# Kernel tuning notes

Measured on AMD Instinct MI355X. Metric: run time of the kernel, lower is better.

## Reference

```python
import jax, jax.numpy as jnp
import numpy as np

N_NODES = 50000
N_EDGES = 1600000
NODE_IN = 128
EDGE_IN = 16
HID = 64

def _glorot(key, shape):
    fan_in = shape[1]
    return jax.random.normal(key, shape, dtype=jnp.float32) / jnp.sqrt(jnp.float32(fan_in))

def setup_inputs() -> dict:
    key = jax.random.key(0)
    ks = jax.random.split(key, 12)
    x = jax.random.normal(ks[0], (N_NODES, NODE_IN), dtype=jnp.float32)
    edge_index = jax.random.randint(ks[1], (2, N_EDGES), 0, N_NODES, dtype=jnp.int64)
    edge_attr = jax.random.normal(ks[2], (N_EDGES, EDGE_IN), dtype=jnp.float32)
    # SAGEConv1: lin_l (neighbor aggr, with bias) and lin_r (root, no bias)
    W1l = _glorot(ks[3], (NODE_IN, HID)); b1l = jnp.zeros((HID,), jnp.float32)
    W1r = _glorot(ks[4], (NODE_IN, HID))
    # SAGEConv2
    W2l = _glorot(ks[5], (HID, HID)); b2l = jnp.zeros((HID,), jnp.float32)
    W2r = _glorot(ks[6], (HID, HID))
    # edge MLP: Linear(2*HID+EDGE_IN, HID) -> ReLU -> Linear(HID, 1)
    Wm1 = _glorot(ks[7], (2 * HID + EDGE_IN, HID)); bm1 = jnp.zeros((HID,), jnp.float32)
    Wm2 = _glorot(ks[8], (HID, 1)); bm2 = jnp.zeros((1,), jnp.float32)
    return {"x": x, "edge_attr": edge_attr,
            "W1l": W1l, "b1l": b1l, "W1r": W1r,
            "W2l": W2l, "b2l": b2l, "W2r": W2r,
            "Wm1": Wm1, "bm1": bm1, "Wm2": Wm2, "bm2": bm2,
            "edge_index": edge_index}

def _sage_conv(h, src, dst, Wl, bl, Wr, n_nodes):
    # mean aggregation of source-node messages at destination nodes
    agg = jax.ops.segment_sum(h[src], dst, num_segments=n_nodes)  # [N, d]
    deg = jax.ops.segment_sum(jnp.ones((src.shape[0],), h.dtype), dst, num_segments=n_nodes)
    mean = agg / jnp.maximum(deg, 1.0)[:, None]
    return mean @ Wl + bl + h @ Wr

def reference(x, edge_attr, W1l, b1l, W1r, W2l, b2l, W2r, Wm1, bm1, Wm2, bm2, edge_index):
    src, dst = edge_index[0], edge_index[1]
    n = x.shape[0]
    h = jax.nn.relu(_sage_conv(x, src, dst, W1l, b1l, W1r, n))
    h = jax.nn.relu(_sage_conv(h, src, dst, W2l, b2l, W2r, n))
    ef = jnp.concatenate([h[src], h[dst], edge_attr], axis=1)  # [E, 2*HID+EDGE_IN]
    hid = jax.nn.relu(ef @ Wm1 + bm1)
    out = hid @ Wm2 + bm2  # [E, 1]
    return jax.nn.sigmoid(out)[:, 0]
```

## Files before the change

### kernel.cpp

```cpp
#include <hip/hip_runtime.h>
#include <hip/hip_bf16.h>
#include <math.h>

#define N_NODES 50000
#define N_EDGES 1600000
#define NODE_IN 128
#define HID 64
#define NODEF (N_NODES * HID)
#define EBLK 64
#define MM1_BLOCKS 1563
#define DEG_BLOCKS 6250
#define NWIN 4
#define SCAN_BLOCKS 49

typedef __hip_bfloat16 bf16;
typedef _Float16 half2t __attribute__((ext_vector_type(2)));

__device__ __forceinline__ float bf2f(bf16 v) { return __bfloat162float(v); }
__device__ __forceinline__ bf16 f2bf(float v) { return __float2bfloat16(v); }

__global__ __launch_bounds__(256) void deg_count_i(const int* __restrict__ dst,
                                                   int* __restrict__ degi, int E) {
    int e = blockIdx.x * blockDim.x + threadIdx.x;
    if (e < E) atomicAdd(&degi[dst[e]], 1);
}

__global__ __launch_bounds__(1024) void scan_blocks(const int* __restrict__ degi,
                                                    int* __restrict__ partial) {
    __shared__ int wsum[16];
    const int t = threadIdx.x;
    const int i = blockIdx.x * 1024 + t;
    const int lane = t & 63, w = t >> 6;
    int v = (i < N_NODES) ? degi[i] : 0;
#pragma unroll
    for (int d = 32; d; d >>= 1) v += __shfl_xor(v, d, 64);
    if (lane == 0) wsum[w] = v;
    __syncthreads();
    if (t == 0) {
        int s = 0;
#pragma unroll
        for (int k = 0; k < 16; ++k) s += wsum[k];
        partial[blockIdx.x] = s;
    }
}

__global__ __launch_bounds__(64) void scan_tops(const int* __restrict__ partial,
                                                int* __restrict__ base) {
    const int t = threadIdx.x;
    int v = (t < SCAN_BLOCKS) ? partial[t] : 0;
    int inc = v;
#pragma unroll
    for (int d = 1; d < 64; d <<= 1) {
        int u = __shfl_up(inc, d, 64);
        if (t >= d) inc += u;
    }
    if (t < SCAN_BLOCKS) base[t] = inc - v;
}

__global__ __launch_bounds__(1024) void scan_final(const int* __restrict__ degi,
                                                   const int* __restrict__ base,
                                                   int* __restrict__ off,
                                                   int* __restrict__ cursor) {
    __shared__ int wsum[16];
    const int t = threadIdx.x;
    const int i = blockIdx.x * 1024 + t;
    const int lane = t & 63, w = t >> 6;
    int v = (i < N_NODES) ? degi[i] : 0;
    int inc = v;
#pragma unroll
    for (int d = 1; d < 64; d <<= 1) {
        int u = __shfl_up(inc, d, 64);
        if (lane >= d) inc += u;
    }
    if (lane == 63) wsum[w] = inc;
    __syncthreads();
    if (w == 0) {
        int s = (lane < 16) ? wsum[lane] : 0;
#pragma unroll
        for (int d = 1; d < 16; d <<= 1) {
            int u = __shfl_up(s, d, 64);
            if (lane >= d) s += u;
        }
        if (lane < 16) wsum[lane] = s;
    }
    __syncthreads();
    const int wbase = (w > 0) ? wsum[w - 1] : 0;
    const int excl = base[blockIdx.x] + wbase + inc - v;
    if (i < N_NODES) { off[i] = excl; cursor[i] = excl; }
    if (i == N_NODES) off[i] = excl;
}

__global__ __launch_bounds__(256) void conv1_fill(const float* __restrict__ in,
                                                  const float* __restrict__ Wa,
                                                  const float* __restrict__ Wb,
                                                  bf16* __restrict__ out1,
                                                  float* __restrict__ out2,
                                                  const int* __restrict__ src,
                                                  const int* __restrict__ dst,
                                                  int* __restrict__ cursor,
                                                  int* __restrict__ csr, int N) {
    constexpr int K = 128, ROWS = 32, PAD = 36;
    __shared__ float xs[K * PAD];
    const int bid = blockIdx.x;
    if (bid >= MM1_BLOCKS) {
        int fb = bid - MM1_BLOCKS;
        int w = fb / DEG_BLOCKS;
        int chunk = fb % DEG_BLOCKS;
        int e = chunk * 256 + threadIdx.x;
        int d = dst[e];
        int lo = w * (N_NODES / NWIN);
        int hi = lo + (N_NODES / NWIN);
        if (d >= lo && d < hi) {
            int p = atomicAdd(&cursor[d], 1);
            csr[p] = src[e];
        }
        return;
    }
    const int row0 = bid * ROWS;
    const int ty = threadIdx.x >> 6;
    const int col = threadIdx.x & 63;
    for (int i = threadIdx.x; i < ROWS * K; i += 256) {
        int r = i / K, c = i % K;
        int row = row0 + r;
        xs[c * PAD + r] = (row < N) ? in[(size_t)row * K + c] : 0.f;
    }
    __syncthreads();
    float a1[8], a2[8];
#pragma unroll
    for (int m = 0; m < 8; ++m) { a1[m] = 0.f; a2[m] = 0.f; }
#pragma unroll 4
    for (int k = 0; k < K; ++k) {
        const float4* xr = (const float4*)(xs + k * PAD + ty * 8);
        float4 xa = xr[0], xb = xr[1];
        float wa = Wa[k * 64 + col];
        float wb = Wb[k * 64 + col];
        a1[0] = fmaf(xa.x, wa, a1[0]); a2[0] = fmaf(xa.x, wb, a2[0]);
        a1[1] = fmaf(xa.y, wa, a1[1]); a2[1] = fmaf(xa.y, wb, a2[1]);
        a1[2] = fmaf(xa.z, wa, a1[2]); a2[2] = fmaf(xa.z, wb, a2[2]);
        a1[3] = fmaf(xa.w, wa, a1[3]); a2[3] = fmaf(xa.w, wb, a2[3]);
        a1[4] = fmaf(xb.x, wa, a1[4]); a2[4] = fmaf(xb.x, wb, a2[4]);
        a1[5] = fmaf(xb.y, wa, a1[5]); a2[5] = fmaf(xb.y, wb, a2[5]);
        a1[6] = fmaf(xb.z, wa, a1[6]); a2[6] = fmaf(xb.z, wb, a2[6]);
        a1[7] = fmaf(xb.w, wa, a1[7]); a2[7] = fmaf(xb.w, wb, a2[7]);
    }
#pragma unroll
    for (int m = 0; m < 8; ++m) {
        int row = row0 + ty * 8 + m;
        if (row < N) {
            unsigned idx = ((unsigned)row << 6) + col;
            out1[idx] = f2bf(a1[m]);
            out2[idx] = a2[m];
        }
    }
}

template <bool OUT1_BF, bool OUT2_BF>
__global__ __launch_bounds__(256) void gather_mm(const bf16* __restrict__ y,
                                                 const float* __restrict__ r,
                                                 const int* __restrict__ csr,
                                                 const int* __restrict__ off,
                                                 const float* __restrict__ bias,
                                                 const float* __restrict__ Wa,
                                                 const float* __restrict__ Wb,
                                                 void* __restrict__ out1v,
                                                 void* __restrict__ out2v, int N) {
    constexpr int K = 64, ROWS = 16, PAD = 20, IDXCAP = 256;
    __shared__ float xs[K * PAD];
    __shared__ int   idx_s[4][IDXCAP];
    const int row0 = blockIdx.x * ROWS;
    const int j  = threadIdx.x & 63;
    const int wv = threadIdx.x >> 6;
    const float bj = bias[j];

    const int nbase = row0 + wv * 4;
    int offs[5];
#pragma unroll
    for (int i = 0; i < 5; ++i) offs[i] = off[nbase + i];
    const int segS = offs[0];
    const int len = offs[4] - segS;
    int* idx_w = idx_s[wv];
    const bool useLds = (len <= IDXCAP);
    if (useLds) {
        for (int i = j; i < len; i += 64)
            idx_w[i] = csr[segS + i];
    }

    for (int m = 0; m < 4; ++m) {
        int lr = wv * 4 + m;
        int node = row0 + lr;
        float acc = 0.f;
        int deg = offs[m + 1] - offs[m];
        if (useLds) {
            int k = offs[m] - segS, s1 = offs[m + 1] - segS;
            for (; k + 15 < s1; k += 16) {
                int sidx[16];
#pragma unroll
                for (int u = 0; u < 16; ++u) sidx[u] = idx_w[k + u];
                float v[16];
#pragma unroll
                for (int u = 0; u < 16; ++u) v[u] = bf2f(y[((unsigned)sidx[u] << 6) + j]);
                float s = 0.f;
#pragma unroll
                for (int u = 0; u < 16; ++u) s += v[u];
                acc += s;
            }
            for (; k + 3 < s1; k += 4) {
                int sa = idx_w[k], sb = idx_w[k + 1], sc = idx_w[k + 2], sd = idx_w[k + 3];
                float va = bf2f(y[((unsigned)sa << 6) + j]);
                float vb = bf2f(y[((unsigned)sb << 6) + j]);
                float vc = bf2f(y[((unsigned)sc << 6) + j]);
                float vd = bf2f(y[((unsigned)sd << 6) + j]);
                acc += (va + vb) + (vc + vd);
            }
            for (; k < s1; ++k)
                acc += bf2f(y[((unsigned)idx_w[k] << 6) + j]);
        } else {
            int k = offs[m], s1 = offs[m + 1];
            for (; k + 15 < s1; k += 16) {
                int sidx[16];
#pragma unroll
                for (int u = 0; u < 16; ++u) sidx[u] = csr[k + u];
                float v[16];
#pragma unroll
                for (int u = 0; u < 16; ++u) v[u] = bf2f(y[((unsigned)sidx[u] << 6) + j]);
                float s = 0.f;
#pragma unroll
                for (int u = 0; u < 16; ++u) s += v[u];
                acc += s;
            }
            for (; k + 3 < s1; k += 4) {
                int sa = csr[k], sb = csr[k + 1], sc = csr[k + 2], sd = csr[k + 3];
                float va = bf2f(y[((unsigned)sa << 6) + j]);
                float vb = bf2f(y[((unsigned)sb << 6) + j]);
                float vc = bf2f(y[((unsigned)sc << 6) + j]);
                float vd = bf2f(y[((unsigned)sd << 6) + j]);
                acc += (va + vb) + (vc + vd);
            }
            for (; k < s1; ++k)
                acc += bf2f(y[((unsigned)csr[k] << 6) + j]);
        }
        float mean = acc / fmaxf((float)deg, 1.f);
        float val = fmaxf(mean + bj + r[((unsigned)node << 6) + j], 0.f);
        xs[j * PAD + lr] = val;
    }
    __syncthreads();

    float a1[4], a2[4];
#pragma unroll
    for (int m = 0; m < 4; ++m) { a1[m] = 0.f; a2[m] = 0.f; }
#pragma unroll 4
    for (int k = 0; k < K; ++k) {
        const float4 xa = *(const float4*)(xs + k * PAD + wv * 4);
        float wa = Wa[k * 64 + j];
        float wb = Wb[k * 64 + j];
        a1[0] = fmaf(xa.x, wa, a1[0]); a2[0] = fmaf(xa.x, wb, a2[0]);
        a1[1] = fmaf(xa.y, wa, a1[1]); a2[1] = fmaf(xa.y, wb, a2[1]);
        a1[2] = fmaf(xa.z, wa, a1[2]); a2[2] = fmaf(xa.z, wb, a2[2]);
        a1[3] = fmaf(xa.w, wa, a1[3]); a2[3] = fmaf(xa.w, wb, a2[3]);
    }
#pragma unroll
    for (int m = 0; m < 4; ++m) {
        int row = row0 + wv * 4 + m;
        if (row < N) {
            unsigned idx = ((unsigned)row << 6) + j;
            if (OUT1_BF) ((bf16*)out1v)[idx] = f2bf(a1[m]);
            else         ((float*)out1v)[idx] = a1[m];
            if (OUT2_BF) ((bf16*)out2v)[idx] = f2bf(a2[m]);
            else         ((float*)out2v)[idx] = a2[m];
        }
    }
}

__device__ __forceinline__ float merge_pair(float lo, float hi, int o, bool bit) {
    float keep = bit ? hi : lo;
    float send = bit ? lo : hi;
    return keep + __shfl_xor(send, o, 64);
}

__global__ __launch_bounds__(256) void edge_fused(const bf16* __restrict__ aE,
                                                  const bf16* __restrict__ bE,
                                                  const float* __restrict__ ea,
                                                  const float* __restrict__ Wbot,
                                                  const float* __restrict__ bm1,
                                                  const float* __restrict__ wm2,
                                                  const float* __restrict__ bm2,
                                                  const int* __restrict__ src,
                                                  const int* __restrict__ dst,
                                                  float* __restrict__ out) {
    __shared__ unsigned ea_s[EBLK * 8];
    __shared__ int      sd_s[2 * EBLK];
    const int t   = threadIdx.x;
    const int eb0 = blockIdx.x * EBLK;
    const int j   = t & 63;
    const int wv  = t >> 6;

    {
        const float2* eaf2 = (const float2*)(ea + (size_t)eb0 * 16);
        for (int i = t; i < EBLK * 8; i += 256) {
            float2 f = eaf2[i];
            half2t p;
            p.x = (_Float16)f.x;
            p.y = (_Float16)f.y;
            ea_s[i] = __builtin_bit_cast(unsigned, p);
        }
    }
    if (t < 2 * EBLK)
        sd_s[t] = (t < EBLK) ? src[eb0 + t] : dst[eb0 + t - EBLK];

    half2t wh[8];
#pragma unroll
    for (int kk = 0; kk < 8; ++kk) {
        wh[kk].x = (_Float16)Wbot[(2 * kk) * 64 + j];
        wh[kk].y = (_Float16)Wbot[(2 * kk + 1) * 64 + j];
    }
    const float bm1c = bm1[j];
    const float wm2c = wm2[j];
    const float bm2c = bm2[0];
    const bool b5 = (j & 32) != 0, b4 = (j & 16) != 0, b3 = (j & 8) != 0;
    __syncthreads();

    const ushort* aU = (const ushort*)aE;
    const ushort* bU = (const ushort*)bE;

    for (int g = 0; g < 2; ++g) {
        const int ebase = wv * 16 + g * 8;
        ushort av[8], bv[8];
#pragma unroll
        for (int u = 0; u < 8; ++u) {
            int e = ebase + u;
            av[u] = aU[((unsigned)sd_s[e] << 6) + j];
            bv[u] = bU[((unsigned)sd_s[EBLK + e] << 6) + j];
        }
        float p[8];
#pragma unroll
        for (int u = 0; u < 8; ++u) {
            const uint4* er = (const uint4*)(ea_s + (ebase + u) * 8);
            uint4 qa = er[0], qb = er[1];
            float v = bm1c;
            v = __builtin_amdgcn_fdot2(__builtin_bit_cast(half2t, qa.x), wh[0], v, false);
            v = __builtin_amdgcn_fdot2(__builtin_bit_cast(half2t, qa.y), wh[1], v, false);
            v = __builtin_amdgcn_fdot2(__builtin_bit_cast(half2t, qa.z), wh[2], v, false);
            v = __builtin_amdgcn_fdot2(__builtin_bit_cast(half2t, qa.w), wh[3], v, false);
            v = __builtin_amdgcn_fdot2(__builtin_bit_cast(half2t, qb.x), wh[4], v, false);
            v = __builtin_amdgcn_fdot2(__builtin_bit_cast(half2t, qb.y), wh[5], v, false);
            v = __builtin_amdgcn_fdot2(__builtin_bit_cast(half2t, qb.z), wh[6], v, false);
            v = __builtin_amdgcn_fdot2(__builtin_bit_cast(half2t, qb.w), wh[7], v, false);
            bf16 ab = *(const bf16*)&av[u];
            bf16 bb = *(const bf16*)&bv[u];
            v += bf2f(ab) + bf2f(bb);
            p[u] = fmaxf(v, 0.f) * wm2c;
        }
        float q0 = merge_pair(p[0], p[1], 32, b5);
        float q1 = merge_pair(p[2], p[3], 32, b5);
        float q2 = merge_pair(p[4], p[5], 32, b5);
        float q3 = merge_pair(p[6], p[7], 32, b5);
        float r0 = merge_pair(q0, q1, 16, b4);
        float r1 = merge_pair(q2, q3, 16, b4);
        float s  = merge_pair(r0, r1, 8, b3);
        s += __shfl_xor(s, 4, 64);
        s += __shfl_xor(s, 2, 64);
        s += __shfl_xor(s, 1, 64);
        if ((j & 7) == 0) {
            int m = 4 * ((j >> 3) & 1) + 2 * ((j >> 4) & 1) + ((j >> 5) & 1);
            out[eb0 + ebase + m] = 1.f / (1.f + __expf(-(s + bm2c)));
        }
    }
}

extern "C" void kernel_launch(void* const* d_in, const int* in_sizes, int n_in,
                              void* d_out, int out_size, void* d_ws, size_t ws_size,
                              hipStream_t stream) {
    const float* x         = (const float*)d_in[0];
    const float* edge_attr = (const float*)d_in[1];
    const float* W1l       = (const float*)d_in[2];
    const float* b1l       = (const float*)d_in[3];
    const float* W1r       = (const float*)d_in[4];
    const float* W2l       = (const float*)d_in[5];
    const float* b2l       = (const float*)d_in[6];
    const float* W2r       = (const float*)d_in[7];
    const float* Wm1       = (const float*)d_in[8];
    const float* bm1       = (const float*)d_in[9];
    const float* Wm2       = (const float*)d_in[10];
    const float* bm2       = (const float*)d_in[11];
    const int*   ei        = (const int*)d_in[12];
    const int*   src       = ei;
    const int*   dst       = ei + N_EDGES;
    float* out = (float*)d_out;

    int*   degi    = (int*)d_ws;
    int*   off     = degi + 50176;
    int*   cursor  = off + 50432;
    int*   partial = cursor + 50000;
    int*   base    = cursor + 50064;
    int*   csr     = cursor + 50176;
    bf16*  bfA     = (bf16*)(csr + N_EDGES);
    bf16*  bfB     = bfA + NODEF;
    bf16*  bfC     = bfB + NODEF;
    float* fR      = (float*)(bfC + NODEF);
    float* fR2     = fR + NODEF;

    const int N = N_NODES, E = N_EDGES;
    const int gmGrid = (N + 15) / 16;
    const int efGrid = E / EBLK;

    hipMemsetAsync(degi, 0, N_NODES * sizeof(int), stream);
    deg_count_i<<<DEG_BLOCKS, 256, 0, stream>>>(dst, degi, E);
    scan_blocks<<<SCAN_BLOCKS, 1024, 0, stream>>>(degi, partial);
    scan_tops<<<1, 64, 0, stream>>>(partial, base);
    scan_final<<<SCAN_BLOCKS, 1024, 0, stream>>>(degi, base, off, cursor);

    conv1_fill<<<MM1_BLOCKS + NWIN * DEG_BLOCKS, 256, 0, stream>>>(
        x, W1l, W1r, bfA, fR, src, dst, cursor, csr, N);

    gather_mm<true, false><<<gmGrid, 256, 0, stream>>>(
        bfA, fR, csr, off, b1l, W2l, W2r, bfB, fR2, N);

    gather_mm<true, true><<<gmGrid, 256, 0, stream>>>(
        bfB, fR2, csr, off, b2l, Wm1, Wm1 + 64 * 64, bfA, bfC, N);

    edge_fused<<<efGrid, 256, 0, stream>>>(bfA, bfC, edge_attr, Wm1 + 128 * 64,
                                           bm1, Wm2, bm2, src, dst, out);
}
```

Baseline: 344.9 us.

## Fuse degree count into conv1 GEMM, split CSR fill, use readlane indices in edge kernel

The degree-count atomics now run in the same launch as the first dense transform, and the windowed CSR fill moves to its own kernel with twice as many destination windows. In the edge MLP kernel, src/dst indices are loaded per wave into registers and broadcast with readlane instead of being staged through shared memory. The intent is to overlap the degree pass with the GEMM, improve atomic locality in the fill, and cut LDS traffic in the edge kernel. The cost is one extra launch, and the fill now reads dst eight times instead of four.

```diff
diff --git a/kernel.cpp b/kernel.cpp
--- a/kernel.cpp
+++ b/kernel.cpp
@@ -10,7 +10,7 @@
 #define EBLK 64
 #define MM1_BLOCKS 1563
 #define DEG_BLOCKS 6250
-#define NWIN 4
+#define NWIN 8
 #define SCAN_BLOCKS 49
 
 typedef __hip_bfloat16 bf16;
@@ -19,101 +19,20 @@
 __device__ __forceinline__ float bf2f(bf16 v) { return __bfloat162float(v); }
 __device__ __forceinline__ bf16 f2bf(float v) { return __float2bfloat16(v); }
 
-__global__ __launch_bounds__(256) void deg_count_i(const int* __restrict__ dst,
-                                                   int* __restrict__ degi, int E) {
-    int e = blockIdx.x * blockDim.x + threadIdx.x;
-    if (e < E) atomicAdd(&degi[dst[e]], 1);
-}
-
-__global__ __launch_bounds__(1024) void scan_blocks(const int* __restrict__ degi,
-                                                    int* __restrict__ partial) {
-    __shared__ int wsum[16];
-    const int t = threadIdx.x;
-    const int i = blockIdx.x * 1024 + t;
-    const int lane = t & 63, w = t >> 6;
-    int v = (i < N_NODES) ? degi[i] : 0;
-#pragma unroll
-    for (int d = 32; d; d >>= 1) v += __shfl_xor(v, d, 64);
-    if (lane == 0) wsum[w] = v;
-    __syncthreads();
-    if (t == 0) {
-        int s = 0;
-#pragma unroll
-        for (int k = 0; k < 16; ++k) s += wsum[k];
-        partial[blockIdx.x] = s;
-    }
-}
-
-__global__ __launch_bounds__(64) void scan_tops(const int* __restrict__ partial,
-                                                int* __restrict__ base) {
-    const int t = threadIdx.x;
-    int v = (t < SCAN_BLOCKS) ? partial[t] : 0;
-    int inc = v;
-#pragma unroll
-    for (int d = 1; d < 64; d <<= 1) {
-        int u = __shfl_up(inc, d, 64);
-        if (t >= d) inc += u;
-    }
-    if (t < SCAN_BLOCKS) base[t] = inc - v;
-}
-
-__global__ __launch_bounds__(1024) void scan_final(const int* __restrict__ degi,
-                                                   const int* __restrict__ base,
-                                                   int* __restrict__ off,
-                                                   int* __restrict__ cursor) {
-    __shared__ int wsum[16];
-    const int t = threadIdx.x;
-    const int i = blockIdx.x * 1024 + t;
-    const int lane = t & 63, w = t >> 6;
-    int v = (i < N_NODES) ? degi[i] : 0;
-    int inc = v;
-#pragma unroll
-    for (int d = 1; d < 64; d <<= 1) {
-        int u = __shfl_up(inc, d, 64);
-        if (lane >= d) inc += u;
-    }
-    if (lane == 63) wsum[w] = inc;
-    __syncthreads();
-    if (w == 0) {
-        int s = (lane < 16) ? wsum[lane] : 0;
-#pragma unroll
-        for (int d = 1; d < 16; d <<= 1) {
-            int u = __shfl_up(s, d, 64);
-            if (lane >= d) s += u;
-        }
-        if (lane < 16) wsum[lane] = s;
-    }
-    __syncthreads();
-    const int wbase = (w > 0) ? wsum[w - 1] : 0;
-    const int excl = base[blockIdx.x] + wbase + inc - v;
-    if (i < N_NODES) { off[i] = excl; cursor[i] = excl; }
-    if (i == N_NODES) off[i] = excl;
-}
-
-__global__ __launch_bounds__(256) void conv1_fill(const float* __restrict__ in,
-                                                  const float* __restrict__ Wa,
-                                                  const float* __restrict__ Wb,
-                                                  bf16* __restrict__ out1,
-                                                  float* __restrict__ out2,
-                                                  const int* __restrict__ src,
-                                                  const int* __restrict__ dst,
-                                                  int* __restrict__ cursor,
-                                                  int* __restrict__ csr, int N) {
+__global__ __launch_bounds__(256) void conv1_and_deg(const float* __restrict__ in,
+                                                     const float* __restrict__ Wa,
+                                                     const float* __restrict__ Wb,
+                                                     bf16* __restrict__ out1,
+                                                     float* __restrict__ out2,
+                                                     const int* __restrict__ dst,
+                                                     int* __restrict__ degi,
+                                                     int N, int E) {
     constexpr int K = 128, ROWS = 32, PAD = 36;
     __shared__ float xs[K * PAD];
     const int bid = blockIdx.x;
     if (bid >= MM1_BLOCKS) {
-        int fb = bid - MM1_BLOCKS;
-        int w = fb / DEG_BLOCKS;
-        int chunk = fb % DEG_BLOCKS;
-        int e = chunk * 256 + threadIdx.x;
-        int d = dst[e];
-        int lo = w * (N_NODES / NWIN);
-        int hi = lo + (N_NODES / NWIN);
-        if (d >= lo && d < hi) {
-            int p = atomicAdd(&cursor[d], 1);
-            csr[p] = src[e];
-        }
+        int e = (bid - MM1_BLOCKS) * 256 + threadIdx.x;
+        if (e < E) atomicAdd(&degi[dst[e]], 1);
         return;
     }
     const int row0 = bid * ROWS;
@@ -151,6 +70,87 @@
             out1[idx] = f2bf(a1[m]);
             out2[idx] = a2[m];
         }
+    }
+}
+
+__global__ __launch_bounds__(1024) void scan_blocks(const int* __restrict__ degi,
+                                                    int* __restrict__ partial) {
+    __shared__ int wsum[16];
+    const int t = threadIdx.x;
+    const int i = blockIdx.x * 1024 + t;
+    const int lane = t & 63, w = t >> 6;
+    int v = (i < N_NODES) ? degi[i] : 0;
+#pragma unroll
+    for (int d = 32; d; d >>= 1) v += __shfl_xor(v, d, 64);
+    if (lane == 0) wsum[w] = v;
+    __syncthreads();
+    if (t == 0) {
+        int s = 0;
+#pragma unroll
+        for (int k = 0; k < 16; ++k) s += wsum[k];
+        partial[blockIdx.x] = s;
+    }
+}
+
+__global__ __launch_bounds__(64) void scan_tops(const int* __restrict__ partial,
+                                                int* __restrict__ base) {
+    const int t = threadIdx.x;
+    int v = (t < SCAN_BLOCKS) ? partial[t] : 0;
+    int inc = v;
+#pragma unroll
+    for (int d = 1; d < 64; d <<= 1) {
+        int u = __shfl_up(inc, d, 64);
+        if (t >= d) inc += u;
+    }
+    if (t < SCAN_BLOCKS) base[t] = inc - v;
+}
+
+__global__ __launch_bounds__(1024) void scan_final(const int* __restrict__ degi,
+                                                   const int* __restrict__ base,
+                                                   int* __restrict__ off,
+                                                   int* __restrict__ cursor) {
+    __shared__ int wsum[16];
+    const int t = threadIdx.x;
+    const int i = blockIdx.x * 1024 + t;
+    const int lane = t & 63, w = t >> 6;
+    int v = (i < N_NODES) ? degi[i] : 0;
+    int inc = v;
+#pragma unroll
+    for (int d = 1; d < 64; d <<= 1) {
+        int u = __shfl_up(inc, d, 64);
+        if (lane >= d) inc += u;
+    }
+    if (lane == 63) wsum[w] = inc;
+    __syncthreads();
+    if (w == 0) {
+        int s = (lane < 16) ? wsum[lane] : 0;
+#pragma unroll
+        for (int d = 1; d < 16; d <<= 1) {
+            int u = __shfl_up(s, d, 64);
+            if (lane >= d) s += u;
+        }
+        if (lane < 16) wsum[lane] = s;
+    }
+    __syncthreads();
+    const int wbase = (w > 0) ? wsum[w - 1] : 0;
+    const int excl = base[blockIdx.x] + wbase + inc - v;
+    if (i < N_NODES) { off[i] = excl; cursor[i] = excl; }
+    if (i == N_NODES) off[i] = excl;
+}
+
+__global__ __launch_bounds__(256) void fill_csr_win(const int* __restrict__ src,
+                                                    const int* __restrict__ dst,
+                                                    int* __restrict__ cursor,
+                                                    int* __restrict__ csr) {
+    int w = blockIdx.x / DEG_BLOCKS;
+    int chunk = blockIdx.x % DEG_BLOCKS;
+    int e = chunk * 256 + threadIdx.x;
+    int d = dst[e];
+    int lo = w * (N_NODES / NWIN);
+    int hi = lo + (N_NODES / NWIN);
+    if (d >= lo && d < hi) {
+        int p = atomicAdd(&cursor[d], 1);
+        csr[p] = src[e];
     }
 }
 
@@ -288,7 +288,6 @@
                                                   const int* __restrict__ dst,
                                                   float* __restrict__ out) {
     __shared__ unsigned ea_s[EBLK * 8];
-    __shared__ int      sd_s[2 * EBLK];
     const int t   = threadIdx.x;
     const int eb0 = blockIdx.x * EBLK;
     const int j   = t & 63;
@@ -304,8 +303,10 @@
             ea_s[i] = __builtin_bit_cast(unsigned, p);
         }
     }
-    if (t < 2 * EBLK)
-        sd_s[t] = (t < EBLK) ? src[eb0 + t] : dst[eb0 + t - EBLK];
+
+    const int ebw = eb0 + wv * 16;
+    const int vsrc = src[ebw + (j & 15)];
+    const int vdst = dst[ebw + (j & 15)];
 
     half2t wh[8];
 #pragma unroll
@@ -322,14 +323,16 @@
     const ushort* aU = (const ushort*)aE;
     const ushort* bU = (const ushort*)bE;
 
+#pragma unroll
     for (int g = 0; g < 2; ++g) {
         const int ebase = wv * 16 + g * 8;
         ushort av[8], bv[8];
 #pragma unroll
         for (int u = 0; u < 8; ++u) {
-            int e = ebase + u;
-            av[u] = aU[((unsigned)sd_s[e] << 6) + j];
-            bv[u] = bU[((unsigned)sd_s[EBLK + e] << 6) + j];
+            int s = __builtin_amdgcn_readlane(vsrc, g * 8 + u);
+            int d = __builtin_amdgcn_readlane(vdst, g * 8 + u);
+            av[u] = aU[((unsigned)s << 6) + j];
+            bv[u] = bU[((unsigned)d << 6) + j];
         }
         float p[8];
 #pragma unroll
@@ -404,13 +407,14 @@
     const int efGrid = E / EBLK;
 
     hipMemsetAsync(degi, 0, N_NODES * sizeof(int), stream);
-    deg_count_i<<<DEG_BLOCKS, 256, 0, stream>>>(dst, degi, E);
+    conv1_and_deg<<<MM1_BLOCKS + DEG_BLOCKS, 256, 0, stream>>>(
+        x, W1l, W1r, bfA, fR, dst, degi, N, E);
+
     scan_blocks<<<SCAN_BLOCKS, 1024, 0, stream>>>(degi, partial);
     scan_tops<<<1, 64, 0, stream>>>(partial, base);
     scan_final<<<SCAN_BLOCKS, 1024, 0, stream>>>(degi, base, off, cursor);
 
-    conv1_fill<<<MM1_BLOCKS + NWIN * DEG_BLOCKS, 256, 0, stream>>>(
-        x, W1l, W1r, bfA, fR, src, dst, cursor, csr, N);
+    fill_csr_win<<<NWIN * DEG_BLOCKS, 256, 0, stream>>>(src, dst, cursor, csr);
 
     gather_mm<true, false><<<gmGrid, 256, 0, stream>>>(
         bfA, fR, csr, off, b1l, W2l, W2r, bfB, fR2, N);
```

Result: no change. 351.3 us (+1.8%).

## Use MFMA 16x16x16 for edge-attr projection in fused edge MLP kernel

Applied to the files above, without the earlier changes.

Replaces the per-lane fdot2 chain that projects the 16 edge attributes through Wm1's bottom rows with four MFMA 16x16x16 f16 instructions per wave, each wave covering 16 edges. The gather of the precomputed per-node projections and the ReLU/second-layer reduction are reorganised to match the MFMA output layout. The old cross-lane merge tree is replaced by 16-lane shuffles, and src/dst indices are now read from registers via shuffles instead of shared memory. Gathers become 4 strided bf16 loads per lane rather than one contiguous row per lane, which may reduce coalescing.

```diff
diff --git a/kernel.cpp b/kernel.cpp
--- a/kernel.cpp
+++ b/kernel.cpp
@@ -15,6 +15,8 @@
 
 typedef __hip_bfloat16 bf16;
 typedef _Float16 half2t __attribute__((ext_vector_type(2)));
+typedef _Float16 half4t __attribute__((ext_vector_type(4)));
+typedef float f32x4 __attribute__((ext_vector_type(4)));
 
 __device__ __forceinline__ float bf2f(bf16 v) { return __bfloat162float(v); }
 __device__ __forceinline__ bf16 f2bf(float v) { return __float2bfloat16(v); }
@@ -271,12 +273,6 @@
     }
 }
 
-__device__ __forceinline__ float merge_pair(float lo, float hi, int o, bool bit) {
-    float keep = bit ? hi : lo;
-    float send = bit ? lo : hi;
-    return keep + __shfl_xor(send, o, 64);
-}
-
 __global__ __launch_bounds__(256) void edge_fused(const bf16* __restrict__ aE,
                                                   const bf16* __restrict__ bE,
                                                   const float* __restrict__ ea,
@@ -287,12 +283,13 @@
                                                   const int* __restrict__ src,
                                                   const int* __restrict__ dst,
                                                   float* __restrict__ out) {
-    __shared__ unsigned ea_s[EBLK * 8];
-    __shared__ int      sd_s[2 * EBLK];
+    __shared__ __align__(16) unsigned ea_s[EBLK * 8];
     const int t   = threadIdx.x;
     const int eb0 = blockIdx.x * EBLK;
     const int j   = t & 63;
     const int wv  = t >> 6;
+    const int lo  = j & 15;
+    const int hi  = j >> 4;
 
     {
         const float2* eaf2 = (const float2*)(ea + (size_t)eb0 * 16);
@@ -304,66 +301,66 @@
             ea_s[i] = __builtin_bit_cast(unsigned, p);
         }
     }
-    if (t < 2 * EBLK)
-        sd_s[t] = (t < EBLK) ? src[eb0 + t] : dst[eb0 + t - EBLK];
-
-    half2t wh[8];
-#pragma unroll
-    for (int kk = 0; kk < 8; ++kk) {
-        wh[kk].x = (_Float16)Wbot[(2 * kk) * 64 + j];
-        wh[kk].y = (_Float16)Wbot[(2 * kk + 1) * 64 + j];
-    }
-    const float bm1c = bm1[j];
-    const float wm2c = wm2[j];
+
+    half4t wb[4];
+#pragma unroll
+    for (int m = 0; m < 4; ++m)
+#pragma unroll
+        for (int i = 0; i < 4; ++i)
+            wb[m][i] = (_Float16)Wbot[(hi * 4 + i) * 64 + 16 * m + lo];
+    float bm1c[4], wm2c[4];
+#pragma unroll
+    for (int m = 0; m < 4; ++m) {
+        bm1c[m] = bm1[16 * m + lo];
+        wm2c[m] = wm2[16 * m + lo];
+    }
     const float bm2c = bm2[0];
-    const bool b5 = (j & 32) != 0, b4 = (j & 16) != 0, b3 = (j & 8) != 0;
-    __syncthreads();
+
+    const int ebw = eb0 + wv * 16;
+    const int vsrc = src[ebw + lo];
+    const int vdst = dst[ebw + lo];
+    __syncthreads();
+
+    const uint2 a2v = *(const uint2*)(ea_s + (wv * 16 + lo) * 8 + hi * 2);
+    const half4t a = __builtin_bit_cast(half4t, a2v);
+
+    f32x4 acc[4];
+#pragma unroll
+    for (int m = 0; m < 4; ++m)
+        acc[m] = (f32x4){bm1c[m], bm1c[m], bm1c[m], bm1c[m]};
+#pragma unroll
+    for (int m = 0; m < 4; ++m)
+        acc[m] = __builtin_amdgcn_mfma_f32_16x16x16f16(a, wb[m], acc[m], 0, 0, 0);
 
     const ushort* aU = (const ushort*)aE;
     const ushort* bU = (const ushort*)bE;
-
-    for (int g = 0; g < 2; ++g) {
-        const int ebase = wv * 16 + g * 8;
-        ushort av[8], bv[8];
-#pragma unroll
-        for (int u = 0; u < 8; ++u) {
-            int e = ebase + u;
-            av[u] = aU[((unsigned)sd_s[e] << 6) + j];
-            bv[u] = bU[((unsigned)sd_s[EBLK + e] << 6) + j];
-        }
-        float p[8];
-#pragma unroll
-        for (int u = 0; u < 8; ++u) {
-            const uint4* er = (const uint4*)(ea_s + (ebase + u) * 8);
-            uint4 qa = er[0], qb = er[1];
-            float v = bm1c;
-            v = __builtin_amdgcn_fdot2(__builtin_bit_cast(half2t, qa.x), wh[0], v, false);
-            v = __builtin_amdgcn_fdot2(__builtin_bit_cast(half2t, qa.y), wh[1], v, false);
-            v = __builtin_amdgcn_fdot2(__builtin_bit_cast(half2t, qa.z), wh[2], v, false);
-            v = __builtin_amdgcn_fdot2(__builtin_bit_cast(half2t, qa.w), wh[3], v, false);
-            v = __builtin_amdgcn_fdot2(__builtin_bit_cast(half2t, qb.x), wh[4], v, false);
-            v = __builtin_amdgcn_fdot2(__builtin_bit_cast(half2t, qb.y), wh[5], v, false);
-            v = __builtin_amdgcn_fdot2(__builtin_bit_cast(half2t, qb.z), wh[6], v, false);
-            v = __builtin_amdgcn_fdot2(__builtin_bit_cast(half2t, qb.w), wh[7], v, false);
-            bf16 ab = *(const bf16*)&av[u];
-            bf16 bb = *(const bf16*)&bv[u];
-            v += bf2f(ab) + bf2f(bb);
-            p[u] = fmaxf(v, 0.f) * wm2c;
-        }
-        float q0 = merge_pair(p[0], p[1], 32, b5);
-        float q1 = merge_pair(p[2], p[3], 32, b5);
-        float q2 = merge_pair(p[4], p[5], 32, b5);
-        float q3 = merge_pair(p[6], p[7], 32, b5);
-        float r0 = merge_pair(q0, q1, 16, b4);
-        float r1 = merge_pair(q2, q3, 16, b4);
-        float s  = merge_pair(r0, r1, 8, b3);
-        s += __shfl_xor(s, 4, 64);
-        s += __shfl_xor(s, 2, 64);
-        s += __shfl_xor(s, 1, 64);
-        if ((j & 7) == 0) {
-            int m = 4 * ((j >> 3) & 1) + 2 * ((j >> 4) & 1) + ((j >> 5) & 1);
-            out[eb0 + ebase + m] = 1.f / (1.f + __expf(-(s + bm2c)));
-        }
+    float esum[4];
+#pragma unroll
+    for (int r = 0; r < 4; ++r) {
+        int s = __shfl(vsrc, hi * 4 + r, 16);
+        int d = __shfl(vdst, hi * 4 + r, 16);
+        const ushort* ap = aU + ((unsigned)s << 6) + lo;
+        const ushort* bp = bU + ((unsigned)d << 6) + lo;
+        ushort au[4], bu[4];
+#pragma unroll
+        for (int m = 0; m < 4; ++m) { au[m] = ap[16 * m]; bu[m] = bp[16 * m]; }
+        float sum = 0.f;
+#pragma unroll
+        for (int m = 0; m < 4; ++m) {
+            float v = acc[m][r] + bf2f(*(const bf16*)&au[m]) + bf2f(*(const bf16*)&bu[m]);
+            sum = fmaf(fmaxf(v, 0.f), wm2c[m], sum);
+        }
+        esum[r] = sum;
+    }
+#pragma unroll
+    for (int o = 1; o < 16; o <<= 1) {
+#pragma unroll
+        for (int r = 0; r < 4; ++r) esum[r] += __shfl_xor(esum[r], o, 16);
+    }
+    if (lo == 0) {
+#pragma unroll
+        for (int r = 0; r < 4; ++r)
+            out[ebw + hi * 4 + r] = 1.f / (1.f + __expf(-(esum[r] + bm2c)));
     }
 }
 
```

Measured after the change: 325.6 us (median of 2 runs). 5.6% less time.
